# Kernel optimization log

Measured on AMD Instinct MI355X. Metric: run time of the kernel, lower is better.

The kernel has to match this reference:

```python
import jax, jax.numpy as jnp
import numpy as np

N_NODES = 50000
N_EDGES = 500000
HID = 256
LAYERS = 15
IN_CH = 2
EPS = 1e-5


def setup_inputs() -> dict:
    key = jax.random.key(0)
    ks = jax.random.split(key, 16)
    s = 0.02
    x = jax.random.normal(ks[0], (N_NODES, IN_CH), dtype=jnp.float32)
    edge_index = jax.random.randint(ks[1], (2, N_EDGES), 0, N_NODES, dtype=jnp.int32)
    # torch-style Linear weights: [out_features, in_features]
    W_in = jax.random.normal(ks[2], (HID, IN_CH), dtype=jnp.float32) * s
    Wrel = jax.random.normal(ks[3], (LAYERS, HID, HID), dtype=jnp.float32) * s
    brel = jnp.zeros((LAYERS, HID), dtype=jnp.float32)
    Wroot = jax.random.normal(ks[4], (LAYERS, HID, HID), dtype=jnp.float32) * s
    gamma = jnp.ones((LAYERS, HID), dtype=jnp.float32)
    beta = jnp.zeros((LAYERS, HID), dtype=jnp.float32)
    W1 = jax.random.normal(ks[5], (HID, 2 * HID), dtype=jnp.float32) * s
    b1 = jnp.zeros((HID,), dtype=jnp.float32)
    W2 = jax.random.normal(ks[6], (HID, HID), dtype=jnp.float32) * s
    b2 = jnp.zeros((HID,), dtype=jnp.float32)
    W3 = jax.random.normal(ks[7], (1, HID), dtype=jnp.float32) * s
    b3 = jnp.zeros((1,), dtype=jnp.float32)
    return {"x": x, "edge_index": edge_index, "W_in": W_in, "Wrel": Wrel,
            "brel": brel, "Wroot": Wroot, "gamma": gamma, "beta": beta,
            "W1": W1, "b1": b1, "W2": W2, "b2": b2, "W3": W3, "b3": b3}


def reference(x, edge_index, W_in, Wrel, brel, Wroot, gamma, beta,
              W1, b1, W2, b2, W3, b3):
    n = x.shape[0]
    src, dst = edge_index[0], edge_index[1]
    h = x @ W_in.T  # input_fc, no bias -> [N, HID]

    def layer(carry, p):
        Wr, br, Wo, g, bt = p
        # GraphConv (aggr='add'): lin_rel(sum_j x_j) + lin_root(x_i)
        agg = jax.ops.segment_sum(carry[src], dst, num_segments=n)
        out = agg @ Wr.T + br + carry @ Wo.T
        # BatchNorm1d, training-mode batch stats (biased var)
        mean = out.mean(axis=0)
        var = out.var(axis=0)
        out = (out - mean) * jax.lax.rsqrt(var + EPS) * g + bt
        return carry + jax.nn.relu(out), None

    h, _ = jax.lax.scan(layer, h, (Wrel, brel, Wroot, gamma, beta))

    # edge MLP on cat([x[row], x[col]])
    e = jnp.concatenate([h[src], h[dst]], axis=-1)  # [E, 2*HID]
    z = jax.nn.relu(e @ W1.T + b1)
    z = jax.nn.relu(z @ W2.T + b2)
    return jax.nn.sigmoid(z @ W3.T + b3)  # [E, 1]
```

## Files before the change

kernel.cpp:

```cpp
#include <hip/hip_runtime.h>
#include <cstdint>
#include <cstddef>

#define HID 256

typedef __bf16 bf16;
typedef __bf16 bf16x4 __attribute__((ext_vector_type(4)));
typedef __bf16 bf16x8 __attribute__((ext_vector_type(8)));
typedef float f32x4 __attribute__((ext_vector_type(4)));


__global__ void k_zero_i32(int* __restrict__ p, int n) {
  int i = blockIdx.x * blockDim.x + threadIdx.x;
  if (i < n) p[i] = 0;
}

__global__ void k_hist(const int* __restrict__ ei, int* __restrict__ deg, int E) {
  int i = blockIdx.x * blockDim.x + threadIdx.x;
  if (i < E) atomicAdd(&deg[ei[E + i]], 1);
}

__global__ void k_scan1(const int* __restrict__ deg, int* __restrict__ offs,
                        int* __restrict__ bsums, int n) {
  __shared__ int sh[1024];
  int i = blockIdx.x * 1024 + threadIdx.x;
  int v = (i < n) ? deg[i] : 0;
  sh[threadIdx.x] = v;
  __syncthreads();
  for (int d = 1; d < 1024; d <<= 1) {
    int t = (threadIdx.x >= (unsigned)d) ? sh[threadIdx.x - d] : 0;
    __syncthreads();
    sh[threadIdx.x] += t;
    __syncthreads();
  }
  if (i < n) offs[i] = sh[threadIdx.x] - v;
  if (threadIdx.x == 1023) bsums[blockIdx.x] = sh[1023];
}

__global__ void k_scan2(int* __restrict__ bsums, int nb) {
  if (threadIdx.x == 0 && blockIdx.x == 0) {
    int run = 0;
    for (int b = 0; b < nb; ++b) { int t = bsums[b]; bsums[b] = run; run += t; }
  }
}

__global__ void k_scan3(int* __restrict__ offs, int* __restrict__ cursor,
                        const int* __restrict__ bsums, int n, int E) {
  int i = blockIdx.x * 1024 + threadIdx.x;
  if (i < n) { int o = offs[i] + bsums[blockIdx.x]; offs[i] = o; cursor[i] = o; }
  if (i == 0) offs[n] = E;
}

__global__ void k_fill(const int* __restrict__ ei, int* __restrict__ cursor,
                       int* __restrict__ csr, int* __restrict__ edst,
                       int* __restrict__ eperm, int E) {
  int i = blockIdx.x * blockDim.x + threadIdx.x;
  if (i < E) {
    int s = ei[i], d = ei[E + i];
    int pos = atomicAdd(&cursor[d], 1);
    csr[pos] = s;
    edst[pos] = d;
    eperm[pos] = i;
  }
}


__global__ void k_pack(const float* __restrict__ W, bf16* __restrict__ P,
                       int OUT, int K, int count) {
  int g = blockIdx.x * blockDim.x + threadIdx.x;
  int total = count * OUT * (K >> 3);
  if (g >= total) return;
  int lane = g & 63;
  int rest = g >> 6;
  int KT = K >> 5;
  int kt = rest % KT;
  int rest2 = rest / KT;
  int OT = OUT >> 4;
  int tile = rest2 % OT;
  int mat = rest2 / OT;
  const float* src = W + (size_t)mat * OUT * K +
                     (size_t)(tile * 16 + (lane & 15)) * K + kt * 32 + (lane >> 4) * 8;
  bf16* dst = P + (size_t)g * 8;
#pragma unroll
  for (int j = 0; j < 8; ++j) dst[j] = (bf16)src[j];
}


__global__ __launch_bounds__(256) void k_input_fc(
    const float* __restrict__ x, const float* __restrict__ Win,
    bf16* __restrict__ hb, float* __restrict__ sums0, int N) {
  int gid = blockIdx.x * blockDim.x + threadIdx.x;
  if (blockIdx.x == 0) { sums0[threadIdx.x] = 0.f; sums0[256 + threadIdx.x] = 0.f; }
  int total = N * HID;
  int stride = gridDim.x * blockDim.x;
  for (int idx = gid; idx < total; idx += stride) {
    int node = idx >> 8, c = idx & 255;
    float v = x[2 * node] * Win[2 * c] + x[2 * node + 1] * Win[2 * c + 1];
    hb[idx] = (bf16)v;
  }
}


__global__ __launch_bounds__(256) void k_aggregate(
    const bf16* __restrict__ hb, const int* __restrict__ offs,
    const int* __restrict__ csr, bf16* __restrict__ aggb, int N) {
  int gwave = (int)((blockIdx.x * blockDim.x + threadIdx.x) >> 6);
  int lane = threadIdx.x & 63;
  int node = gwave * 2 + (lane >> 5);
  int l32 = lane & 31;
  if (node >= N) return;
  int e0 = offs[node], e1 = offs[node + 1];
  float a[8] = {};
  int e = e0;
  for (; e + 3 < e1; e += 4) {
    int s0 = csr[e], s1 = csr[e + 1], s2 = csr[e + 2], s3 = csr[e + 3];
    bf16x8 v0 = *(const bf16x8*)(hb + (size_t)s0 * HID + l32 * 8);
    bf16x8 v1 = *(const bf16x8*)(hb + (size_t)s1 * HID + l32 * 8);
    bf16x8 v2 = *(const bf16x8*)(hb + (size_t)s2 * HID + l32 * 8);
    bf16x8 v3 = *(const bf16x8*)(hb + (size_t)s3 * HID + l32 * 8);
#pragma unroll
    for (int k = 0; k < 8; ++k)
      a[k] += ((float)v0[k] + (float)v1[k]) + ((float)v2[k] + (float)v3[k]);
  }
  for (; e < e1; ++e) {
    int s0 = csr[e];
    bf16x8 v0 = *(const bf16x8*)(hb + (size_t)s0 * HID + l32 * 8);
#pragma unroll
    for (int k = 0; k < 8; ++k) a[k] += (float)v0[k];
  }
  bf16x8 o;
#pragma unroll
  for (int k = 0; k < 8; ++k) o[k] = (bf16)a[k];
  *(bf16x8*)(aggb + (size_t)node * HID + l32 * 8) = o;
}


__global__ __launch_bounds__(256) void k_layer_gemm(
    const bf16* __restrict__ aggb, const bf16* __restrict__ hb,
    const bf16* __restrict__ Pr, const bf16* __restrict__ Po,
    const float* __restrict__ bias, bf16* __restrict__ out,
    float* __restrict__ sums, int N) {
  __shared__ __align__(16) bf16 bt[32 * 64 * 8];
  __shared__ float bsum[256], bsq[256];
  int tid = threadIdx.x;
  int wave = tid >> 6, lane = tid & 63;
  int l15 = lane & 15, lq = lane >> 4;
  int m0 = blockIdx.x * 64;
  f32x4 acc[4][4] = {};
  const bf16* PrW = Pr + (size_t)wave * 4 * 8 * 64 * 8;
  const bf16* PoW = Po + (size_t)wave * 4 * 8 * 64 * 8;
  int rr = tid & 63, cb = tid >> 6;
  int sj = rr >> 4, sl = rr & 15;

  for (int phase = 0; phase < 2; ++phase) {
    const bf16* src = phase ? hb : aggb;
    if (phase) __syncthreads();
    {
      int gr = m0 + rr;
      bool ok = gr < N;
#pragma unroll
      for (int it = 0; it < 8; ++it) {
        int c = cb + it * 4;
        bf16x8 v = {};
        if (ok) v = *(const bf16x8*)(src + (size_t)gr * HID + c * 8);
        *(bf16x8*)(&bt[(((c >> 2) * 4 + sj) * 64 + (c & 3) * 16 + sl) * 8]) = v;
      }
    }
    __syncthreads();
    const bf16* PW = phase ? PoW : PrW;
    for (int kt = 0; kt < 8; ++kt) {
      bf16x8 bfr[4];
#pragma unroll
      for (int j = 0; j < 4; ++j)
        bfr[j] = *(const bf16x8*)(&bt[((kt * 4 + j) * 64 + lane) * 8]);
#pragma unroll
      for (int i = 0; i < 4; ++i) {
        bf16x8 afr = *(const bf16x8*)(PW + ((size_t)(i * 8 + kt) * 64 + lane) * 8);
#pragma unroll
        for (int j = 0; j < 4; ++j)
          acc[i][j] = __builtin_amdgcn_mfma_f32_16x16x32_bf16(afr, bfr[j], acc[i][j], 0, 0, 0);
      }
    }
  }

  f32x4 bv[4];
#pragma unroll
  for (int i = 0; i < 4; ++i)
    bv[i] = *(const f32x4*)(bias + wave * 64 + i * 16 + lq * 4);
  float s[4][4] = {}, q[4][4] = {};
#pragma unroll
  for (int j = 0; j < 4; ++j) {
    int gn = m0 + j * 16 + l15;
    bool ok = gn < N;
#pragma unroll
    for (int i = 0; i < 4; ++i) {
      bf16x4 o;
#pragma unroll
      for (int r = 0; r < 4; ++r) {
        float v = acc[i][j][r] + bv[i][r];
        o[r] = (bf16)v;
        if (ok) { s[i][r] += v; q[i][r] += v * v; }
      }
      if (ok) *(bf16x4*)(out + (size_t)gn * HID + wave * 64 + i * 16 + lq * 4) = o;
    }
  }
#pragma unroll
  for (int d = 1; d < 16; d <<= 1) {
#pragma unroll
    for (int i = 0; i < 4; ++i)
#pragma unroll
      for (int r = 0; r < 4; ++r) {
        s[i][r] += __shfl_xor(s[i][r], d, 64);
        q[i][r] += __shfl_xor(q[i][r], d, 64);
      }
  }
  if (l15 == 0) {
#pragma unroll
    for (int i = 0; i < 4; ++i)
#pragma unroll
      for (int r = 0; r < 4; ++r) {
        bsum[wave * 64 + i * 16 + lq * 4 + r] = s[i][r];
        bsq[wave * 64 + i * 16 + lq * 4 + r] = q[i][r];
      }
  }
  __syncthreads();
  atomicAdd(&sums[tid], bsum[tid]);
  atomicAdd(&sums[256 + tid], bsq[tid]);
}


__global__ __launch_bounds__(256) void k_bn_residual(
    const bf16* __restrict__ outb, bf16* __restrict__ hb,
    const float* __restrict__ sums, float* __restrict__ zsums,
    const float* __restrict__ gamma, const float* __restrict__ beta,
    int N, float invN) {
  int t = threadIdx.x;
  if (blockIdx.x == 0) { zsums[t] = 0.f; zsums[256 + t] = 0.f; }
  int cg = (t & 31) * 8;
  int r0 = blockIdx.x * 32 + (t >> 5) * 4;
  float a[8], b[8];
#pragma unroll
  for (int k = 0; k < 8; ++k) {
    int c = cg + k;
    float mean = sums[c] * invN;
    float var = sums[256 + c] * invN - mean * mean;
    float istd = rsqrtf(var + 1e-5f);
    a[k] = istd * gamma[c];
    b[k] = fmaf(-mean, a[k], beta[c]);
  }
  int r1 = min(r0 + 4, N);
  for (int r = r0; r < r1; ++r) {
    size_t idx = (size_t)r * HID + cg;
    bf16x8 ov = *(const bf16x8*)(outb + idx);
    bf16x8 hv = *(const bf16x8*)(hb + idx);
    bf16x8 o;
#pragma unroll
    for (int k = 0; k < 8; ++k) {
      float y = fmaf((float)ov[k], a[k], b[k]);
      y = fmaxf(y, 0.f);
      o[k] = (bf16)((float)hv[k] + y);
    }
    *(bf16x8*)(hb + idx) = o;
  }
}


__global__ __launch_bounds__(256) void k_edge_mlp(
    const bf16* __restrict__ hb, const int* __restrict__ csr,
    const int* __restrict__ edst, const int* __restrict__ eperm,
    const bf16* __restrict__ P1, const float* __restrict__ b1v,
    const bf16* __restrict__ P2, const float* __restrict__ b2v,
    const float* __restrict__ w3, const float* __restrict__ b3,
    float* __restrict__ outp, int E) {
  __shared__ __align__(16) bf16 asp[2][4 * 64 * 8];
  __shared__ __align__(16) bf16 z1f[32 * 64 * 8];
  __shared__ int nd[128];
  __shared__ int oidx[64];
  __shared__ float red[64];
  int tid = threadIdx.x;
  int e0 = blockIdx.x * 64;
  if (tid < 64) {
    int p = e0 + tid;
    nd[tid] = (p < E) ? csr[p] : 0;
    oidx[tid] = (p < E) ? eperm[p] : -1;
  } else if (tid < 128) {
    int p = e0 + (tid - 64);
    nd[tid] = (p < E) ? edst[p] : 0;
  }
  if (tid < 64) red[tid] = 0.f;
  __syncthreads();
  int wave = tid >> 6, lane = tid & 63;
  int l15 = lane & 15, lq = lane >> 4;
  int sr = tid >> 2, sq = tid & 3;
  int slot = ((sr >> 4) * 64 + sq * 16 + (sr & 15)) * 8;

  f32x4 acc[4][4] = {};
  const bf16* P1W = P1 + (size_t)wave * 4 * 16 * 64 * 8;
  {
    int node = nd[sr];
    bf16x8 v = *(const bf16x8*)(hb + (size_t)node * HID + sq * 8);
    *(bf16x8*)(&asp[0][slot]) = v;
  }
  __syncthreads();
  for (int ks = 0; ks < 16; ++ks) {
    bf16x8 vn;
    bool has = (ks + 1) < 16;
    if (has) {
      int node = nd[((ks + 1) >> 3) * 64 + sr];
      vn = *(const bf16x8*)(hb + (size_t)node * HID + ((ks + 1) & 7) * 32 + sq * 8);
    }
    const bf16* cur = asp[ks & 1];
    bf16x8 bfr[4];
#pragma unroll
    for (int j = 0; j < 4; ++j)
      bfr[j] = *(const bf16x8*)(&cur[(j * 64 + lane) * 8]);
#pragma unroll
    for (int i = 0; i < 4; ++i) {
      bf16x8 wf = *(const bf16x8*)(P1W + ((size_t)(i * 16 + ks) * 64 + lane) * 8);
#pragma unroll
      for (int j = 0; j < 4; ++j)
        acc[i][j] = __builtin_amdgcn_mfma_f32_16x16x32_bf16(wf, bfr[j], acc[i][j], 0, 0, 0);
    }
    if (has) *(bf16x8*)(&asp[(ks + 1) & 1][slot]) = vn;
    __syncthreads();
  }
  {
    f32x4 b1i[4];
#pragma unroll
    for (int i = 0; i < 4; ++i)
      b1i[i] = *(const f32x4*)(b1v + wave * 64 + i * 16 + lq * 4);
#pragma unroll
    for (int j = 0; j < 4; ++j) {
#pragma unroll
      for (int i = 0; i < 4; ++i) {
        bf16x4 o;
#pragma unroll
        for (int r = 0; r < 4; ++r)
          o[r] = (bf16)fmaxf(acc[i][j][r] + b1i[i][r], 0.f);
        int kt = wave * 2 + (i >> 1);
        int slt = l15 + 16 * ((i & 1) * 2 + (lq >> 1));
        *(bf16x4*)(&z1f[((j * 8 + kt) * 64 + slt) * 8 + (lq & 1) * 4]) = o;
      }
    }
  }
  __syncthreads();

  f32x4 acc2[4][4] = {};
  const bf16* P2W = P2 + (size_t)wave * 4 * 8 * 64 * 8;
  for (int ks = 0; ks < 8; ++ks) {
    bf16x8 zf[4];
#pragma unroll
    for (int j = 0; j < 4; ++j)
      zf[j] = *(const bf16x8*)(&z1f[((j * 8 + ks) * 64 + lane) * 8]);
#pragma unroll
    for (int i = 0; i < 4; ++i) {
      bf16x8 wf = *(const bf16x8*)(P2W + ((size_t)(i * 8 + ks) * 64 + lane) * 8);
#pragma unroll
      for (int j = 0; j < 4; ++j)
        acc2[i][j] = __builtin_amdgcn_mfma_f32_16x16x32_bf16(wf, zf[j], acc2[i][j], 0, 0, 0);
    }
  }

  f32x4 b2i[4], w3i[4];
#pragma unroll
  for (int i = 0; i < 4; ++i) {
    b2i[i] = *(const f32x4*)(b2v + wave * 64 + i * 16 + lq * 4);
    w3i[i] = *(const f32x4*)(w3 + wave * 64 + i * 16 + lq * 4);
  }
  float sj2[4] = {};
#pragma unroll
  for (int j = 0; j < 4; ++j)
#pragma unroll
    for (int i = 0; i < 4; ++i)
#pragma unroll
      for (int r = 0; r < 4; ++r)
        sj2[j] = fmaf(fmaxf(acc2[i][j][r] + b2i[i][r], 0.f), w3i[i][r], sj2[j]);
#pragma unroll
  for (int j = 0; j < 4; ++j) {
    sj2[j] += __shfl_xor(sj2[j], 16, 64);
    sj2[j] += __shfl_xor(sj2[j], 32, 64);
  }
  if (lq == 0) {
#pragma unroll
    for (int j = 0; j < 4; ++j)
      atomicAdd(&red[j * 16 + l15], sj2[j]);
  }
  __syncthreads();
  if (tid < 64) {
    int oi = oidx[tid];
    if (oi >= 0) {
      float logit = red[tid] + b3[0];
      outp[oi] = 1.f / (1.f + expf(-logit));
    }
  }
}


static inline size_t align256(size_t x) { return (x + 255) & ~(size_t)255; }

extern "C" void kernel_launch(void* const* d_in, const int* in_sizes, int n_in,
                              void* d_out, int out_size, void* d_ws, size_t ws_size,
                              hipStream_t stream) {
  const float* x     = (const float*)d_in[0];
  const int*   ei    = (const int*)d_in[1];
  const float* Win   = (const float*)d_in[2];
  const float* Wrel  = (const float*)d_in[3];
  const float* brel  = (const float*)d_in[4];
  const float* Wroot = (const float*)d_in[5];
  const float* gamma = (const float*)d_in[6];
  const float* beta  = (const float*)d_in[7];
  const float* W1    = (const float*)d_in[8];
  const float* b1    = (const float*)d_in[9];
  const float* W2    = (const float*)d_in[10];
  const float* b2    = (const float*)d_in[11];
  const float* W3    = (const float*)d_in[12];
  const float* b3    = (const float*)d_in[13];

  const int N = in_sizes[0] / 2;
  const int E = in_sizes[1] / 2;
  const int L = in_sizes[3] / (HID * HID);

  char* p = (char*)d_ws;
  auto alloc = [&](size_t bytes) { char* r = p; p += align256(bytes); return r; };
  bf16*  hb    = (bf16*)alloc((size_t)N * HID * 2);
  bf16*  outb  = (bf16*)alloc((size_t)N * HID * 2);
  bf16*  aggb  = (bf16*)alloc((size_t)N * HID * 2);
  bf16*  Prel  = (bf16*)alloc((size_t)L * HID * HID * 2);
  bf16*  Proot = (bf16*)alloc((size_t)L * HID * HID * 2);
  bf16*  P1    = (bf16*)alloc((size_t)HID * 2 * HID * 2);
  bf16*  P2    = (bf16*)alloc((size_t)HID * HID * 2);
  int*   deg   = (int*)alloc((size_t)N * 4);
  int*   offs  = (int*)alloc((size_t)(N + 1) * 4);
  int*   cursor= (int*)alloc((size_t)N * 4);
  int*   csr   = (int*)alloc((size_t)E * 4);
  int*   edst  = (int*)alloc((size_t)E * 4);
  int*   eperm = (int*)alloc((size_t)E * 4);
  int*   bsums = (int*)alloc(64 * 4);
  float* sums  = (float*)alloc(1024 * 4);
  (void)ws_size; (void)n_in; (void)out_size;

  const int nb = (N + 1023) / 1024;

  k_zero_i32<<<(N + 255) / 256, 256, 0, stream>>>(deg, N);
  k_hist<<<(E + 255) / 256, 256, 0, stream>>>(ei, deg, E);
  k_scan1<<<nb, 1024, 0, stream>>>(deg, offs, bsums, N);
  k_scan2<<<1, 64, 0, stream>>>(bsums, nb);
  k_scan3<<<nb, 1024, 0, stream>>>(offs, cursor, bsums, N, E);
  k_fill<<<(E + 255) / 256, 256, 0, stream>>>(ei, cursor, csr, edst, eperm, E);

  {
    int g1 = L * HID * HID / 8;
    k_pack<<<(g1 + 255) / 256, 256, 0, stream>>>(Wrel, Prel, HID, HID, L);
    k_pack<<<(g1 + 255) / 256, 256, 0, stream>>>(Wroot, Proot, HID, HID, L);
    int g2 = HID * 2 * HID / 8;
    k_pack<<<(g2 + 255) / 256, 256, 0, stream>>>(W1, P1, HID, 2 * HID, 1);
    int g3 = HID * HID / 8;
    k_pack<<<(g3 + 255) / 256, 256, 0, stream>>>(W2, P2, HID, HID, 1);
  }

  k_input_fc<<<1024, 256, 0, stream>>>(x, Win, hb, sums, N);

  const float invN = 1.0f / (float)N;
  for (int l = 0; l < L; ++l) {
    int sel = l & 1;
    k_aggregate<<<(N + 7) / 8, 256, 0, stream>>>(hb, offs, csr, aggb, N);
    k_layer_gemm<<<(N + 63) / 64, 256, 0, stream>>>(
        aggb, hb, Prel + (size_t)l * HID * HID, Proot + (size_t)l * HID * HID,
        brel + (size_t)l * HID, outb, sums + sel * 512, N);
    k_bn_residual<<<(N + 31) / 32, 256, 0, stream>>>(
        outb, hb, sums + sel * 512, sums + (1 - sel) * 512,
        gamma + (size_t)l * HID, beta + (size_t)l * HID, N, invN);
  }

  k_edge_mlp<<<(E + 63) / 64, 256, 0, stream>>>(
      hb, csr, edst, eperm, P1, b1, P2, b2, W3, b3, (float*)d_out, E);
}
```

Baseline: 1.970 ms.

## Double edge tile per block in edge MLP and alias gather buffer with z1

The edge MLP kernel now processes 128 edges per block instead of 64. This halves the number of times the P1/P2 weight fragments are reloaded from global memory per edge and doubles the MFMA work per weight load. The separate double-buffered gather tile is removed and its storage is aliased onto the z1 LDS buffer, which keeps shared memory bounded. Each thread now gathers two 16-byte chunks per step and holds twice as many accumulators (4x8 tiles), with launch bounds set to 2 blocks per CU. This raises register pressure and may reduce occupancy.

```diff
diff --git a/kernel.cpp b/kernel.cpp
--- a/kernel.cpp
+++ b/kernel.cpp
@@ -265,63 +265,71 @@
 }
 
 
-__global__ __launch_bounds__(256) void k_edge_mlp(
+__global__ __launch_bounds__(256, 2) void k_edge_mlp(
     const bf16* __restrict__ hb, const int* __restrict__ csr,
     const int* __restrict__ edst, const int* __restrict__ eperm,
     const bf16* __restrict__ P1, const float* __restrict__ b1v,
     const bf16* __restrict__ P2, const float* __restrict__ b2v,
     const float* __restrict__ w3, const float* __restrict__ b3,
     float* __restrict__ outp, int E) {
-  __shared__ __align__(16) bf16 asp[2][4 * 64 * 8];
-  __shared__ __align__(16) bf16 z1f[32 * 64 * 8];
-  __shared__ int nd[128];
-  __shared__ int oidx[64];
-  __shared__ float red[64];
+  __shared__ __align__(16) bf16 z1f[64 * 64 * 8];
+  __shared__ int nd[256];
+  __shared__ int oidx[128];
+  __shared__ float red[128];
   int tid = threadIdx.x;
-  int e0 = blockIdx.x * 64;
-  if (tid < 64) {
-    int p = e0 + tid;
-    nd[tid] = (p < E) ? csr[p] : 0;
-    oidx[tid] = (p < E) ? eperm[p] : -1;
-  } else if (tid < 128) {
-    int p = e0 + (tid - 64);
-    nd[tid] = (p < E) ? edst[p] : 0;
-  }
-  if (tid < 64) red[tid] = 0.f;
-  __syncthreads();
+  int e0 = blockIdx.x * 128;
+  {
+    int p = e0 + (tid & 127);
+    if (tid < 128) {
+      nd[tid] = (p < E) ? csr[p] : 0;
+      oidx[tid] = (p < E) ? eperm[p] : -1;
+      red[tid] = 0.f;
+    } else {
+      nd[tid] = (p < E) ? edst[p] : 0;
+    }
+  }
   int wave = tid >> 6, lane = tid & 63;
   int l15 = lane & 15, lq = lane >> 4;
-  int sr = tid >> 2, sq = tid & 3;
-  int slot = ((sr >> 4) * 64 + sq * 16 + (sr & 15)) * 8;
-
-  f32x4 acc[4][4] = {};
+  int row = tid & 127, half = tid >> 7;
+  int sslotA = ((row >> 4) * 64 + (half * 2) * 16 + (row & 15)) * 8;
+  int sslotB = ((row >> 4) * 64 + (half * 2 + 1) * 16 + (row & 15)) * 8;
+  __syncthreads();
+
+  f32x4 acc[4][8] = {};
   const bf16* P1W = P1 + (size_t)wave * 4 * 16 * 64 * 8;
   {
-    int node = nd[sr];
-    bf16x8 v = *(const bf16x8*)(hb + (size_t)node * HID + sq * 8);
-    *(bf16x8*)(&asp[0][slot]) = v;
+    int node = nd[row];
+    const bf16* rp = hb + (size_t)node * HID + half * 16;
+    *(bf16x8*)(&z1f[sslotA]) = *(const bf16x8*)(rp);
+    *(bf16x8*)(&z1f[sslotB]) = *(const bf16x8*)(rp + 8);
   }
   __syncthreads();
   for (int ks = 0; ks < 16; ++ks) {
-    bf16x8 vn;
+    bf16x8 vn0, vn1;
     bool has = (ks + 1) < 16;
     if (has) {
-      int node = nd[((ks + 1) >> 3) * 64 + sr];
-      vn = *(const bf16x8*)(hb + (size_t)node * HID + ((ks + 1) & 7) * 32 + sq * 8);
-    }
-    const bf16* cur = asp[ks & 1];
-    bf16x8 bfr[4];
-#pragma unroll
-    for (int j = 0; j < 4; ++j)
+      int node = nd[((ks + 1) >> 3) * 128 + row];
+      const bf16* rp = hb + (size_t)node * HID + ((ks + 1) & 7) * 32 + half * 16;
+      vn0 = *(const bf16x8*)(rp);
+      vn1 = *(const bf16x8*)(rp + 8);
+    }
+    const bf16* cur = z1f + (ks & 1) * 4096;
+    bf16x8 bfr[8];
+#pragma unroll
+    for (int j = 0; j < 8; ++j)
       bfr[j] = *(const bf16x8*)(&cur[(j * 64 + lane) * 8]);
 #pragma unroll
     for (int i = 0; i < 4; ++i) {
       bf16x8 wf = *(const bf16x8*)(P1W + ((size_t)(i * 16 + ks) * 64 + lane) * 8);
 #pragma unroll
-      for (int j = 0; j < 4; ++j)
+      for (int j = 0; j < 8; ++j)
         acc[i][j] = __builtin_amdgcn_mfma_f32_16x16x32_bf16(wf, bfr[j], acc[i][j], 0, 0, 0);
     }
-    if (has) *(bf16x8*)(&asp[(ks + 1) & 1][slot]) = vn;
+    if (has) {
+      bf16* nxt = z1f + ((ks + 1) & 1) * 4096;
+      *(bf16x8*)(&nxt[sslotA]) = vn0;
+      *(bf16x8*)(&nxt[sslotB]) = vn1;
+    }
     __syncthreads();
   }
   {
@@ -330,7 +338,7 @@
     for (int i = 0; i < 4; ++i)
       b1i[i] = *(const f32x4*)(b1v + wave * 64 + i * 16 + lq * 4);
 #pragma unroll
-    for (int j = 0; j < 4; ++j) {
+    for (int j = 0; j < 8; ++j) {
 #pragma unroll
       for (int i = 0; i < 4; ++i) {
         bf16x4 o;
@@ -345,18 +353,18 @@
   }
   __syncthreads();
 
-  f32x4 acc2[4][4] = {};
+  f32x4 acc2[4][8] = {};
   const bf16* P2W = P2 + (size_t)wave * 4 * 8 * 64 * 8;
   for (int ks = 0; ks < 8; ++ks) {
-    bf16x8 zf[4];
-#pragma unroll
-    for (int j = 0; j < 4; ++j)
+    bf16x8 zf[8];
+#pragma unroll
+    for (int j = 0; j < 8; ++j)
       zf[j] = *(const bf16x8*)(&z1f[((j * 8 + ks) * 64 + lane) * 8]);
 #pragma unroll
     for (int i = 0; i < 4; ++i) {
       bf16x8 wf = *(const bf16x8*)(P2W + ((size_t)(i * 8 + ks) * 64 + lane) * 8);
 #pragma unroll
-      for (int j = 0; j < 4; ++j)
+      for (int j = 0; j < 8; ++j)
         acc2[i][j] = __builtin_amdgcn_mfma_f32_16x16x32_bf16(wf, zf[j], acc2[i][j], 0, 0, 0);
     }
   }
@@ -367,26 +375,26 @@
     b2i[i] = *(const f32x4*)(b2v + wave * 64 + i * 16 + lq * 4);
     w3i[i] = *(const f32x4*)(w3 + wave * 64 + i * 16 + lq * 4);
   }
-  float sj2[4] = {};
-#pragma unroll
-  for (int j = 0; j < 4; ++j)
+  float sj2[8] = {};
+#pragma unroll
+  for (int j = 0; j < 8; ++j)
 #pragma unroll
     for (int i = 0; i < 4; ++i)
 #pragma unroll
       for (int r = 0; r < 4; ++r)
         sj2[j] = fmaf(fmaxf(acc2[i][j][r] + b2i[i][r], 0.f), w3i[i][r], sj2[j]);
 #pragma unroll
-  for (int j = 0; j < 4; ++j) {
+  for (int j = 0; j < 8; ++j) {
     sj2[j] += __shfl_xor(sj2[j], 16, 64);
     sj2[j] += __shfl_xor(sj2[j], 32, 64);
   }
   if (lq == 0) {
 #pragma unroll
-    for (int j = 0; j < 4; ++j)
+    for (int j = 0; j < 8; ++j)
       atomicAdd(&red[j * 16 + l15], sj2[j]);
   }
   __syncthreads();
-  if (tid < 64) {
+  if (tid < 128) {
     int oi = oidx[tid];
     if (oi >= 0) {
       float logit = red[tid] + b3[0];
@@ -472,6 +480,6 @@
         gamma + (size_t)l * HID, beta + (size_t)l * HID, N, invN);
   }
 
-  k_edge_mlp<<<(E + 63) / 64, 256, 0, stream>>>(
+  k_edge_mlp<<<(E + 127) / 128, 256, 0, stream>>>(
       hb, csr, edst, eperm, P1, b1, P2, b2, W3, b3, (float*)d_out, E);
 }
```

Result: faster. 1.928 ms (-2.1%).
